# Kernel tuning notes

Measured on AMD Instinct MI355X. Metric: run time of the kernel, lower is better.

## Reference

```python
import jax, jax.numpy as jnp
import numpy as np

N, K, CIN, COUT = 100000, 16, 128, 128
D2 = COUT // 2
EPS = 1e-5


def setup_inputs() -> dict:
    key = jax.random.key(0)
    ks = jax.random.split(key, 12)

    def w(k, shape, fan_in):
        return (jax.random.normal(k, shape, jnp.float32) / np.sqrt(fan_in)).astype(jnp.float32)

    return {
        "xyz": jax.random.normal(ks[0], (N, 3), jnp.float32),
        "x": jax.random.normal(ks[1], (N, CIN), jnp.float32),
        "knn": jax.random.randint(ks[2], (N, K), 0, N, jnp.int32),
        "W": w(ks[3], (CIN, COUT), CIN),            # proj (no bias)
        "m1_w": w(ks[4], (3, D2), 3),                # NCA mlp1
        "m1_b": jnp.zeros((D2,), jnp.float32),
        "m2_w": w(ks[5], (D2, D2), D2),              # NCA mlp2
        "m2_b": jnp.zeros((D2,), jnp.float32),
        "m3a_w": w(ks[6], (COUT, COUT), COUT),       # NCA mlp3[0]
        "m3a_b": jnp.zeros((COUT,), jnp.float32),
        "m3b_w": w(ks[7], (COUT, COUT), COUT),       # NCA mlp3[2]
        "m3b_b": jnp.zeros((COUT,), jnp.float32),
        "gamma": jnp.ones((COUT,), jnp.float32),     # bn.weight (init=1.0)
        "beta": jnp.zeros((COUT,), jnp.float32),     # bn.bias
    }


def reference(xyz, x, knn, W, m1_w, m1_b, m2_w, m2_b, m3a_w, m3a_b, m3b_w, m3b_b, gamma, beta):
    # linear projection of features
    xp = x @ W                                   # (N, C)
    # neighbor gathers (irregular access)
    xs = xp[knn] - xp[:, None, :]                # (N, K, C)
    xyzs = xyz[knn] - xyz[:, None, :]            # (N, K, 3)
    # NCA positional MLP
    p0 = xyzs @ m1_w + m1_b                      # (N, K, C/2)
    p_local = p0.max(axis=1)                     # (N, C/2)
    p1 = p0 @ m2_w + m2_b                        # (N, K, C/2)
    pfeat = jnp.concatenate(
        [p1, jnp.broadcast_to(p_local[:, None, :], p1.shape)], axis=-1
    )                                            # (N, K, C)
    pe = jax.nn.gelu(pfeat @ m3a_w + m3a_b, approximate=False) @ m3b_w + m3b_b
    # add PE, max-aggregate over neighbors
    xs_max = (xs + pe).max(axis=1)               # (N, C)
    # BatchNorm1d (training mode: batch stats, biased variance)
    mean = xs_max.mean(axis=0)
    var = ((xs_max - mean) ** 2).mean(axis=0)
    return (xs_max - mean) / jnp.sqrt(var + EPS) * gamma + beta
```

## Files before the change

kernel.cpp:

```cpp
#include <hip/hip_runtime.h>
#include <hip/hip_bf16.h>
#include <math.h>

#define KNN 16
#define CIN 128
#define COUT 128
#define D2 64
#define EPS 1e-5f

typedef __attribute__((ext_vector_type(8))) short short8;
typedef __attribute__((ext_vector_type(4))) float f32x4;
typedef unsigned int u32;
typedef unsigned short u16;

union S8U { short8 s; u32 u[4]; };

#define MFMA16(a, b, c) __builtin_amdgcn_mfma_f32_16x16x32_bf16((a), (b), (c), 0, 0, 0)

static __device__ __forceinline__ u16 f2bf(float f) {
  __hip_bfloat16 h = __float2bfloat16(f);
  u16 u; __builtin_memcpy(&u, &h, 2); return u;
}
#if __has_builtin(__builtin_amdgcn_cvt_pk_bf16_f32)
static __device__ __forceinline__ u32 pack2(float a, float b) {
  auto r = __builtin_amdgcn_cvt_pk_bf16_f32(a, b);
  u32 u; __builtin_memcpy(&u, &r, 4); return u;
}
#else
static __device__ __forceinline__ u32 pack2(float a, float b) {
  return (u32)f2bf(a) | ((u32)f2bf(b) << 16);
}
#endif
static __device__ __forceinline__ float bf_lo(u32 u) { return __uint_as_float(u << 16); }
static __device__ __forceinline__ float bf_hi(u32 u) { return __uint_as_float(u & 0xffff0000u); }

static __device__ __forceinline__ float gelu_fast(float x) {
  float e = __builtin_amdgcn_exp2f(x * -2.4555331f);
  return x * __builtin_amdgcn_rcpf(1.0f + e);
}

template <int CTRL>
static __device__ __forceinline__ float dppmax(float v) {
  int s = __builtin_bit_cast(int, v);
  int t = __builtin_amdgcn_update_dpp(s, s, CTRL, 0xf, 0xf, true);
  return fmaxf(v, __builtin_bit_cast(float, t));
}
static __device__ __forceinline__ float rowmax16(float v) {
  v = dppmax<0xB1>(v);
  v = dppmax<0x4E>(v);
  v = dppmax<0x141>(v);
  v = dppmax<0x128>(v);
  return v;
}

__global__ __launch_bounds__(256) void k_proj(const float* __restrict__ x,
                                              const float* __restrict__ W,
                                              u32* __restrict__ xp, int n) {
  __shared__ __align__(16) u32 Wf[8192];
  const int t = threadIdx.x;
  for (int idx = t; idx < 8192; idx += 256) {
    int f = idx >> 8, rem = idx & 255;
    int l = rem >> 2, jp = rem & 3;
    int mt = f >> 2, ks = f & 3;
    int qq = l >> 4, mm = l & 15;
    int k = ks * 32 + qq * 8 + jp * 2;
    int c = mt * 16 + mm;
    Wf[idx] = pack2(W[(size_t)k * COUT + c], W[(size_t)(k + 1) * COUT + c]);
  }
  __syncthreads();

  const int wv = t >> 6, l = t & 63;
  const int q = l >> 4, m = l & 15;
  const short8* Wf8 = (const short8*)Wf;

  for (int tile = blockIdx.x * 4 + wv; tile * 16 < n; tile += gridDim.x * 4) {
    int r0 = tile * 16;
    int rr = min(r0 + m, n - 1);
    const float4* xr = (const float4*)(x + (size_t)rr * CIN);
    S8U xf[4];
#pragma unroll
    for (int ks = 0; ks < 4; ks++) {
      float4 a = xr[ks * 8 + q * 2];
      float4 b = xr[ks * 8 + q * 2 + 1];
      xf[ks].u[0] = pack2(a.x, a.y);
      xf[ks].u[1] = pack2(a.z, a.w);
      xf[ks].u[2] = pack2(b.x, b.y);
      xf[ks].u[3] = pack2(b.z, b.w);
    }
    bool ok = (r0 + m) < n;
    size_t rowb = (size_t)(r0 + m) * 64;
#pragma unroll
    for (int mt = 0; mt < 8; mt++) {
      f32x4 acc = {0.f, 0.f, 0.f, 0.f};
      __builtin_amdgcn_s_setprio(1);
#pragma unroll
      for (int ks = 0; ks < 4; ks++)
        acc = MFMA16(Wf8[(mt * 4 + ks) * 64 + l], xf[ks].s, acc);
      __builtin_amdgcn_s_setprio(0);
      if (ok) {
        uint2 v;
        v.x = pack2(acc[0], acc[1]);
        v.y = pack2(acc[2], acc[3]);
        *(uint2*)&xp[rowb + mt * 8 + q * 2] = v;
      }
    }
  }
}

__global__ __launch_bounds__(1024, 4) void k_lfa(
    const float* __restrict__ xyz, const u32* __restrict__ xp,
    const int* __restrict__ knn,
    const float* __restrict__ m1w, const float* __restrict__ m1b,
    const float* __restrict__ m2w, const float* __restrict__ m2b,
    const float* __restrict__ m3aw, const float* __restrict__ m3ab,
    const float* __restrict__ m3bw, const float* __restrict__ m3bb,
    float* __restrict__ xsmax, int n) {
  __shared__ __align__(16) char lds[116992];

  const int t = threadIdx.x, wv = t >> 6, l = t & 63;
  const int q = l >> 4, m = l & 15;

  {
    u32* lds32 = (u32*)lds;
    for (int idx = t; idx < 18432; idx += 1024) {
      int f = idx >> 8, rem = idx & 255;
      int ll = rem >> 2, jp = rem & 3;
      int qq = ll >> 4, mm = ll & 15;
      int j0 = jp * 2;
      float a, b;
      if (f < 8) {
        int mt = f >> 1, s = f & 1;
        const float* p = m2w + (size_t)(s * 32 + qq * 8 + j0) * D2 + mt * 16 + mm;
        a = p[0]; b = p[D2];
      } else if (f < 40) {
        int ff = f - 8; int mt = ff >> 2, s = ff & 3;
        const float* p = m3aw + (size_t)(s * 32 + qq * 8 + j0) * COUT + mt * 16 + mm;
        a = p[0]; b = p[COUT];
      } else {
        int ff = f - 40; int mt = ff >> 2, s = ff & 3;
        const float* p = m3bw + (size_t)(s * 32 + qq * 8 + j0) * COUT + mt * 16 + mm;
        a = p[0]; b = p[COUT];
      }
      lds32[idx] = pack2(a, b);
    }
    if (t < 64) {
      int p = (t & 32) + (t & 7) * 4 + ((t >> 3) & 3);
      ((float4*)(lds + 73728))[p] = make_float4(m1w[t], m1w[64 + t], m1w[128 + t], m1b[t]);
    }
    if (t < 320) {
      float* bias = (float*)(lds + 74752);
      bias[t] = (t < 64) ? m2b[t] : (t < 192) ? m3ab[t - 64] : m3bb[t - 192];
    }
  }
  __syncthreads();

  const char* fr = lds;
  const float4* w14 = (const float4*)(lds + 73728);
  const float* bias = (const float*)(lds + 74752);
  char* sA = lds + 76032 + wv * 2560;
  char* sB = sA + 1280;

  for (int pr = blockIdx.x * 16 + wv; pr * 2 < n; pr += gridDim.x * 16) {
    const int ptA = pr * 2;
    const int ptB = ptA + 1;
    const bool hasB = ptB < n;
    const int ptBc = hasB ? ptB : ptA;
    const int kidA = knn[(size_t)ptA * KNN + m];
    const int kidB = knn[(size_t)ptBc * KNN + m];

    uint2 gA[8], gB[8];
#pragma unroll
    for (int mt = 0; mt < 8; mt++) {
      gA[mt] = *(const uint2*)(xp + (size_t)kidA * 64 + mt * 8 + q * 2);
      gB[mt] = *(const uint2*)(xp + (size_t)kidB * 64 + mt * 8 + q * 2);
    }

    float pxA = xyz[ptA * 3 + 0], pyA = xyz[ptA * 3 + 1], pzA = xyz[ptA * 3 + 2];
    float pxB = xyz[ptBc * 3 + 0], pyB = xyz[ptBc * 3 + 1], pzB = xyz[ptBc * 3 + 2];
    float axA = xyz[kidA * 3 + 0] - pxA, ayA = xyz[kidA * 3 + 1] - pyA, azA = xyz[kidA * 3 + 2] - pzA;
    float axB = xyz[kidB * 3 + 0] - pxB, ayB = xyz[kidB * 3 + 1] - pyB, azB = xyz[kidB * 3 + 2] - pzB;

    float p0A[16], p0B[16];
#pragma unroll
    for (int s = 0; s < 2; s++)
#pragma unroll
      for (int j = 0; j < 8; j++) {
        float4 w = w14[s * 32 + j * 4 + q];
        p0A[s * 8 + j] = fmaf(axA, w.x, fmaf(ayA, w.y, fmaf(azA, w.z, w.w)));
        p0B[s * 8 + j] = fmaf(axB, w.x, fmaf(ayB, w.y, fmaf(azB, w.z, w.w)));
      }
    S8U bp0A[2], bp0B[2], bplA[2], bplB[2];
#pragma unroll
    for (int s = 0; s < 2; s++)
#pragma unroll
      for (int jj = 0; jj < 4; jj++) {
        bp0A[s].u[jj] = pack2(p0A[s * 8 + 2 * jj], p0A[s * 8 + 2 * jj + 1]);
        bp0B[s].u[jj] = pack2(p0B[s * 8 + 2 * jj], p0B[s * 8 + 2 * jj + 1]);
      }
#pragma unroll
    for (int i = 0; i < 16; i++) { p0A[i] = rowmax16(p0A[i]); p0B[i] = rowmax16(p0B[i]); }
#pragma unroll
    for (int s = 0; s < 2; s++)
#pragma unroll
      for (int jj = 0; jj < 4; jj++) {
        bplA[s].u[jj] = pack2(p0A[s * 8 + 2 * jj], p0A[s * 8 + 2 * jj + 1]);
        bplB[s].u[jj] = pack2(p0B[s * 8 + 2 * jj], p0B[s * 8 + 2 * jj + 1]);
      }

    short8 bpfA[2], bpfB[2];
#pragma unroll
    for (int s = 0; s < 2; s++) {
#pragma unroll
      for (int h = 0; h < 2; h++) {
        int mt = 2 * s + h;
        float4 bb = *(const float4*)&bias[mt * 16 + q * 4];
        f32x4 accA = {bb.x, bb.y, bb.z, bb.w};
        f32x4 accB = accA;
        __builtin_amdgcn_s_setprio(1);
#pragma unroll
        for (int ks = 0; ks < 2; ks++) {
          short8 af = *(const short8*)(fr + (mt * 2 + ks) * 1024 + l * 16);
          accA = MFMA16(af, bp0A[ks].s, accA);
          accB = MFMA16(af, bp0B[ks].s, accB);
        }
        __builtin_amdgcn_s_setprio(0);
        uint2 wA; wA.x = pack2(accA[0], accA[1]); wA.y = pack2(accA[2], accA[3]);
        uint2 wB; wB.x = pack2(accB[0], accB[1]); wB.y = pack2(accB[2], accB[3]);
        *(uint2*)(sA + m * 80 + h * 32 + q * 8) = wA;
        *(uint2*)(sB + m * 80 + h * 32 + q * 8) = wB;
      }
      bpfA[s] = *(const short8*)(sA + m * 80 + q * 16);
      bpfB[s] = *(const short8*)(sB + m * 80 + q * 16);
    }

    short8 bgA[4], bgB[4];
#pragma unroll
    for (int s = 0; s < 4; s++) {
#pragma unroll
      for (int h = 0; h < 2; h++) {
        int mt = 2 * s + h;
        float4 bb = *(const float4*)&bias[64 + mt * 16 + q * 4];
        f32x4 accA = {bb.x, bb.y, bb.z, bb.w};
        f32x4 accB = accA;
        __builtin_amdgcn_s_setprio(1);
#pragma unroll
        for (int ks = 0; ks < 4; ks++) {
          short8 af = *(const short8*)(fr + (8 + mt * 4 + ks) * 1024 + l * 16);
          short8 bA = (ks == 0) ? bpfA[0] : (ks == 1) ? bpfA[1] : (ks == 2) ? bplA[0].s : bplA[1].s;
          short8 bB = (ks == 0) ? bpfB[0] : (ks == 1) ? bpfB[1] : (ks == 2) ? bplB[0].s : bplB[1].s;
          accA = MFMA16(af, bA, accA);
          accB = MFMA16(af, bB, accB);
        }
        __builtin_amdgcn_s_setprio(0);
        uint2 wA; wA.x = pack2(gelu_fast(accA[0]), gelu_fast(accA[1]));
        wA.y = pack2(gelu_fast(accA[2]), gelu_fast(accA[3]));
        uint2 wB; wB.x = pack2(gelu_fast(accB[0]), gelu_fast(accB[1]));
        wB.y = pack2(gelu_fast(accB[2]), gelu_fast(accB[3]));
        *(uint2*)(sA + m * 80 + h * 32 + q * 8) = wA;
        *(uint2*)(sB + m * 80 + h * 32 + q * 8) = wB;
      }
      bgA[s] = *(const short8*)(sA + m * 80 + q * 16);
      bgB[s] = *(const short8*)(sB + m * 80 + q * 16);
    }

#pragma unroll
    for (int mt = 0; mt < 8; mt++) {
      float4 bb = *(const float4*)&bias[192 + mt * 16 + q * 4];
      f32x4 accA = {bb.x, bb.y, bb.z, bb.w};
      f32x4 accB = accA;
      __builtin_amdgcn_s_setprio(1);
#pragma unroll
      for (int ks = 0; ks < 4; ks++) {
        short8 af = *(const short8*)(fr + (40 + mt * 4 + ks) * 1024 + l * 16);
        accA = MFMA16(af, bgA[ks], accA);
        accB = MFMA16(af, bgB[ks], accB);
      }
      __builtin_amdgcn_s_setprio(0);
      {
        uint2 sf = *(const uint2*)(xp + (size_t)ptA * 64 + mt * 8 + q * 2);
        float v0 = bf_lo(gA[mt].x) + accA[0];
        float v1 = bf_hi(gA[mt].x) + accA[1];
        float v2 = bf_lo(gA[mt].y) + accA[2];
        float v3 = bf_hi(gA[mt].y) + accA[3];
        v0 = rowmax16(v0); v1 = rowmax16(v1); v2 = rowmax16(v2); v3 = rowmax16(v3);
        if (m == 0) {
          float4 o = make_float4(v0 - bf_lo(sf.x), v1 - bf_hi(sf.x),
                                 v2 - bf_lo(sf.y), v3 - bf_hi(sf.y));
          *(float4*)&xsmax[(size_t)ptA * COUT + mt * 16 + q * 4] = o;
        }
      }
      {
        uint2 sf = *(const uint2*)(xp + (size_t)ptBc * 64 + mt * 8 + q * 2);
        float v0 = bf_lo(gB[mt].x) + accB[0];
        float v1 = bf_hi(gB[mt].x) + accB[1];
        float v2 = bf_lo(gB[mt].y) + accB[2];
        float v3 = bf_hi(gB[mt].y) + accB[3];
        v0 = rowmax16(v0); v1 = rowmax16(v1); v2 = rowmax16(v2); v3 = rowmax16(v3);
        if (hasB && m == 0) {
          float4 o = make_float4(v0 - bf_lo(sf.x), v1 - bf_hi(sf.x),
                                 v2 - bf_lo(sf.y), v3 - bf_hi(sf.y));
          *(float4*)&xsmax[(size_t)ptB * COUT + mt * 16 + q * 4] = o;
        }
      }
    }
  }
}

__global__ __launch_bounds__(256) void k_bnstats(const float* __restrict__ xs,
                                                 float* __restrict__ part, int n) {
  int t = threadIdx.x;
  int c = t & 127;
  int h = t >> 7;
  float s = 0.f, s2 = 0.f;
  for (int r = blockIdx.x * 2 + h; r < n; r += gridDim.x * 2) {
    float v = xs[(size_t)r * COUT + c];
    s += v;
    s2 += v * v;
  }
  __shared__ float red[256];
  red[t] = s;
  __syncthreads();
  if (h == 0) part[blockIdx.x * 256 + c] = s + red[t + 128];
  __syncthreads();
  red[t] = s2;
  __syncthreads();
  if (h == 0) part[blockIdx.x * 256 + 128 + c] = s2 + red[t + 128];
}

__global__ __launch_bounds__(1024) void k_bnfinal(const float* __restrict__ part,
                                                  float* __restrict__ ms,
                                                  int n, int nb) {
  __shared__ float red[2048];
  int t = threadIdx.x;
  int c = t & 127;
  int h = t >> 7;
  float s = 0.f, s2 = 0.f;
  for (int b = h; b < nb; b += 8) {
    s += part[b * 256 + c];
    s2 += part[b * 256 + 128 + c];
  }
  red[t] = s;
  red[1024 + t] = s2;
  __syncthreads();
  if (h == 0) {
#pragma unroll
    for (int k = 1; k < 8; k++) {
      s += red[k * 128 + c];
      s2 += red[1024 + k * 128 + c];
    }
    float inv_n = 1.0f / (float)n;
    float mean = s * inv_n;
    float var = s2 * inv_n - mean * mean;
    ms[c] = mean;
    ms[128 + c] = rsqrtf(var + EPS);
  }
}

__global__ __launch_bounds__(256) void k_bnnorm(const float* __restrict__ xs,
                                                const float* __restrict__ ms,
                                                const float* __restrict__ gamma,
                                                const float* __restrict__ beta,
                                                float* __restrict__ out, int n) {
  size_t i = (size_t)blockIdx.x * 256 + threadIdx.x;
  size_t total4 = (size_t)n * (COUT / 4);
  if (i >= total4) return;
  int c = (int)((i * 4) & (COUT - 1));
  float4 v = ((const float4*)xs)[i];
  float4 mn = *(const float4*)&ms[c];
  float4 iv = *(const float4*)&ms[128 + c];
  float4 gm = *(const float4*)&gamma[c];
  float4 bt = *(const float4*)&beta[c];
  float4 o;
  o.x = (v.x - mn.x) * iv.x * gm.x + bt.x;
  o.y = (v.y - mn.y) * iv.y * gm.y + bt.y;
  o.z = (v.z - mn.z) * iv.z * gm.z + bt.z;
  o.w = (v.w - mn.w) * iv.w * gm.w + bt.w;
  ((float4*)out)[i] = o;
}

extern "C" void kernel_launch(void* const* d_in, const int* in_sizes, int n_in,
                              void* d_out, int out_size, void* d_ws, size_t ws_size,
                              hipStream_t stream) {
  const float* xyz = (const float*)d_in[0];
  const float* x = (const float*)d_in[1];
  const int* knn = (const int*)d_in[2];
  const float* W = (const float*)d_in[3];
  const float* m1w = (const float*)d_in[4];
  const float* m1b = (const float*)d_in[5];
  const float* m2w = (const float*)d_in[6];
  const float* m2b = (const float*)d_in[7];
  const float* m3aw = (const float*)d_in[8];
  const float* m3ab = (const float*)d_in[9];
  const float* m3bw = (const float*)d_in[10];
  const float* m3bb = (const float*)d_in[11];
  const float* gamma = (const float*)d_in[12];
  const float* beta = (const float*)d_in[13];
  float* out = (float*)d_out;

  int n = in_sizes[0] / 3;

  char* ws = (char*)d_ws;
  u32* xp = (u32*)ws;
  size_t o1 = (((size_t)n * 256 + 255) & ~(size_t)255);
  float* xsm = (float*)(ws + o1);
  size_t o2 = o1 + (((size_t)n * 512 + 255) & ~(size_t)255);
  float* part = (float*)(ws + o2);
  size_t o3 = o2 + 524288;
  float* ms = (float*)(ws + o3);

  k_proj<<<512, 256, 0, stream>>>(x, W, xp, n);
  k_lfa<<<256, 1024, 0, stream>>>(xyz, xp, knn, m1w, m1b, m2w, m2b,
                                  m3aw, m3ab, m3bw, m3bb, xsm, n);
  k_bnstats<<<512, 256, 0, stream>>>(xsm, part, n);
  k_bnfinal<<<1, 1024, 0, stream>>>(part, ms, n, 512);
  k_bnnorm<<<(int)(((size_t)n * (COUT / 4) + 255) / 256), 256, 0, stream>>>(
      xsm, ms, gamma, beta, out, n);
}
```

Before: 483.7 us.

## Fuse BatchNorm statistics into LFA kernel via LDS and global atomics

Accumulates per-channel sum and sum-of-squares in LDS with atomics inside the neighbor-aggregation kernel, then flushes each block's partials to global memory with atomicAdd. This removes the separate stats kernel, which re-read the whole xsmax buffer, and leaves a tiny finalize kernel. The partial buffer is zeroed in the projection kernel, whose grid is also doubled. In exchange it adds LDS atomic contention on shared channels and makes the float summation order nondeterministic.

```diff
diff --git a/kernel.cpp b/kernel.cpp
--- a/kernel.cpp
+++ b/kernel.cpp
@@ -55,9 +55,12 @@
 
 __global__ __launch_bounds__(256) void k_proj(const float* __restrict__ x,
                                               const float* __restrict__ W,
-                                              u32* __restrict__ xp, int n) {
+                                              u32* __restrict__ xp,
+                                              float* __restrict__ part, int n) {
+  const int t = threadIdx.x;
+  if (blockIdx.x == 0 && t < 256) part[t] = 0.f;
+
   __shared__ __align__(16) u32 Wf[8192];
-  const int t = threadIdx.x;
   for (int idx = t; idx < 8192; idx += 256) {
     int f = idx >> 8, rem = idx & 255;
     int l = rem >> 2, jp = rem & 3;
@@ -114,8 +117,8 @@
     const float* __restrict__ m2w, const float* __restrict__ m2b,
     const float* __restrict__ m3aw, const float* __restrict__ m3ab,
     const float* __restrict__ m3bw, const float* __restrict__ m3bb,
-    float* __restrict__ xsmax, int n) {
-  __shared__ __align__(16) char lds[116992];
+    float* __restrict__ xsmax, float* __restrict__ part, int n) {
+  __shared__ __align__(16) char lds[118016];
 
   const int t = threadIdx.x, wv = t >> 6, l = t & 63;
   const int q = l >> 4, m = l & 15;
@@ -151,12 +154,14 @@
       float* bias = (float*)(lds + 74752);
       bias[t] = (t < 64) ? m2b[t] : (t < 192) ? m3ab[t - 64] : m3bb[t - 192];
     }
+    if (t < 256) ((float*)(lds + 116992))[t] = 0.f;
   }
   __syncthreads();
 
   const char* fr = lds;
   const float4* w14 = (const float4*)(lds + 73728);
   const float* bias = (const float*)(lds + 74752);
+  float* bn = (float*)(lds + 116992);
   char* sA = lds + 76032 + wv * 2560;
   char* sB = sA + 1280;
 
@@ -287,6 +292,11 @@
           float4 o = make_float4(v0 - bf_lo(sf.x), v1 - bf_hi(sf.x),
                                  v2 - bf_lo(sf.y), v3 - bf_hi(sf.y));
           *(float4*)&xsmax[(size_t)ptA * COUT + mt * 16 + q * 4] = o;
+          int c = mt * 16 + q * 4;
+          atomicAdd(&bn[c + 0], o.x); atomicAdd(&bn[c + 1], o.y);
+          atomicAdd(&bn[c + 2], o.z); atomicAdd(&bn[c + 3], o.w);
+          atomicAdd(&bn[128 + c + 0], o.x * o.x); atomicAdd(&bn[128 + c + 1], o.y * o.y);
+          atomicAdd(&bn[128 + c + 2], o.z * o.z); atomicAdd(&bn[128 + c + 3], o.w * o.w);
         }
       }
       {
@@ -300,60 +310,30 @@
           float4 o = make_float4(v0 - bf_lo(sf.x), v1 - bf_hi(sf.x),
                                  v2 - bf_lo(sf.y), v3 - bf_hi(sf.y));
           *(float4*)&xsmax[(size_t)ptB * COUT + mt * 16 + q * 4] = o;
+          int c = mt * 16 + q * 4;
+          atomicAdd(&bn[c + 0], o.x); atomicAdd(&bn[c + 1], o.y);
+          atomicAdd(&bn[c + 2], o.z); atomicAdd(&bn[c + 3], o.w);
+          atomicAdd(&bn[128 + c + 0], o.x * o.x); atomicAdd(&bn[128 + c + 1], o.y * o.y);
+          atomicAdd(&bn[128 + c + 2], o.z * o.z); atomicAdd(&bn[128 + c + 3], o.w * o.w);
         }
       }
     }
   }
-}
-
-__global__ __launch_bounds__(256) void k_bnstats(const float* __restrict__ xs,
-                                                 float* __restrict__ part, int n) {
-  int t = threadIdx.x;
-  int c = t & 127;
-  int h = t >> 7;
-  float s = 0.f, s2 = 0.f;
-  for (int r = blockIdx.x * 2 + h; r < n; r += gridDim.x * 2) {
-    float v = xs[(size_t)r * COUT + c];
-    s += v;
-    s2 += v * v;
-  }
-  __shared__ float red[256];
-  red[t] = s;
+
   __syncthreads();
-  if (h == 0) part[blockIdx.x * 256 + c] = s + red[t + 128];
-  __syncthreads();
-  red[t] = s2;
-  __syncthreads();
-  if (h == 0) part[blockIdx.x * 256 + 128 + c] = s2 + red[t + 128];
-}
-
-__global__ __launch_bounds__(1024) void k_bnfinal(const float* __restrict__ part,
-                                                  float* __restrict__ ms,
-                                                  int n, int nb) {
-  __shared__ float red[2048];
-  int t = threadIdx.x;
-  int c = t & 127;
-  int h = t >> 7;
-  float s = 0.f, s2 = 0.f;
-  for (int b = h; b < nb; b += 8) {
-    s += part[b * 256 + c];
-    s2 += part[b * 256 + 128 + c];
-  }
-  red[t] = s;
-  red[1024 + t] = s2;
-  __syncthreads();
-  if (h == 0) {
-#pragma unroll
-    for (int k = 1; k < 8; k++) {
-      s += red[k * 128 + c];
-      s2 += red[1024 + k * 128 + c];
-    }
-    float inv_n = 1.0f / (float)n;
-    float mean = s * inv_n;
-    float var = s2 * inv_n - mean * mean;
-    ms[c] = mean;
-    ms[128 + c] = rsqrtf(var + EPS);
-  }
+  if (t < 256) atomicAdd(&part[t], bn[t]);
+}
+
+__global__ void k_bnfinal(const float* __restrict__ part, float* __restrict__ ms,
+                          int n) {
+  int c = threadIdx.x;
+  float s = part[c];
+  float s2 = part[128 + c];
+  float inv_n = 1.0f / (float)n;
+  float mean = s * inv_n;
+  float var = s2 * inv_n - mean * mean;
+  ms[c] = mean;
+  ms[128 + c] = rsqrtf(var + EPS);
 }
 
 __global__ __launch_bounds__(256) void k_bnnorm(const float* __restrict__ xs,
@@ -408,11 +388,10 @@
   size_t o3 = o2 + 524288;
   float* ms = (float*)(ws + o3);
 
-  k_proj<<<512, 256, 0, stream>>>(x, W, xp, n);
+  k_proj<<<1024, 256, 0, stream>>>(x, W, xp, part, n);
   k_lfa<<<256, 1024, 0, stream>>>(xyz, xp, knn, m1w, m1b, m2w, m2b,
-                                  m3aw, m3ab, m3bw, m3bb, xsm, n);
-  k_bnstats<<<512, 256, 0, stream>>>(xsm, part, n);
-  k_bnfinal<<<1, 1024, 0, stream>>>(part, ms, n, 512);
+                                  m3aw, m3ab, m3bw, m3bb, xsm, part, n);
+  k_bnfinal<<<1, 128, 0, stream>>>(part, ms, n);
   k_bnnorm<<<(int)(((size_t)n * (COUT / 4) + 255) / 256), 256, 0, stream>>>(
       xsm, ms, gamma, beta, out, n);
 }
```

Measured after the change: 473.2 us. -2.2%, faster.
